# Performance work log

Measured on AMD Instinct MI355X. Metric: run time of the kernel, lower is better.

The kernel has to match this reference:

```python
import jax, jax.numpy as jnp
import numpy as np

V = 49152   # HEALPix nside=64 sphere: 12*64^2 vertices
B = 16      # batch of maps
DEG = 8     # avg neighbors per vertex
NNZ = V * DEG


def setup_inputs() -> dict:
    key = jax.random.key(0)
    ks = jax.random.split(key, 12)
    x = jax.random.normal(ks[0], (B, V, 1), jnp.float32)
    # COO sparse Laplacian (row-sorted)
    edge_row = jnp.repeat(jnp.arange(V, dtype=jnp.int32), DEG)
    edge_col = jax.random.randint(ks[1], (NNZ,), 0, V, dtype=jnp.int32)
    edge_w = jax.random.normal(ks[2], (NNZ,), jnp.float32) * 0.1

    def w(k, K, fi, fo):
        scale = 1.0 / np.sqrt(fi * K)
        return jax.random.normal(k, (K, fi, fo), jnp.float32) * scale

    return dict(
        x=x, edge_row=edge_row, edge_col=edge_col, edge_w=edge_w,
        w1=w(ks[3], 3, 1, 16),  b1=jnp.zeros((16,), jnp.float32),
        w2=w(ks[4], 3, 16, 64), b2=jnp.zeros((64,), jnp.float32),
        w3=w(ks[5], 3, 64, 16), b3=jnp.zeros((16,), jnp.float32),
        w4=w(ks[6], 1, 16, 1),  b4=jnp.zeros((1,), jnp.float32),
    )


def _spmm(edge_row, edge_col, edge_w, x_vbf):
    # sparse Laplacian @ x ; x_vbf: [V, B, F]
    msg = edge_w[:, None, None] * x_vbf[edge_col]          # [nnz, B, F]
    return jax.ops.segment_sum(msg, edge_row, num_segments=x_vbf.shape[0])


def _cheb_conv(edge_row, edge_col, edge_w, x_vbf, W, b):
    # Chebyshev recursion: x0 = x, x1 = L x, xk = 2 L x_{k-1} - x_{k-2}
    K = W.shape[0]
    xs = [x_vbf]
    if K > 1:
        xs.append(_spmm(edge_row, edge_col, edge_w, x_vbf))
        for _ in range(2, K):
            xs.append(2.0 * _spmm(edge_row, edge_col, edge_w, xs[-1]) - xs[-2])
    xk = jnp.stack(xs)                                     # [K, V, B, Fin]
    return jnp.einsum('kvbi,kio->vbo', xk, W) + b          # [V, B, Fout]


def reference(x, edge_row, edge_col, edge_w, w1, b1, w2, b2, w3, b3, w4, b4):
    h = jnp.transpose(x, (1, 0, 2))                        # [V, B, 1]
    h = jax.nn.relu(_cheb_conv(edge_row, edge_col, edge_w, h, w1, b1))
    h = jax.nn.relu(_cheb_conv(edge_row, edge_col, edge_w, h, w2, b2))
    h = jax.nn.relu(_cheb_conv(edge_row, edge_col, edge_w, h, w3, b3))
    h = _cheb_conv(edge_row, edge_col, edge_w, h, w4, b4)  # K=1 pointwise
    return jnp.transpose(h, (1, 0, 2))                     # [B, V, 1]
```

## Files before the change

kernel.cpp:

```cpp
#include <hip/hip_runtime.h>

#define V_N 49152
#define B_N 16
#define DEG 8

typedef __bf16 bf16x8 __attribute__((ext_vector_type(8)));
typedef __bf16 bf16x4 __attribute__((ext_vector_type(4)));
typedef __bf16 bf16x2 __attribute__((ext_vector_type(2)));
typedef float f32x4 __attribute__((ext_vector_type(4)));


template <int G>
__global__ __launch_bounds__(256) void k_transpose_g(const float* __restrict__ x,
                                                     float* __restrict__ xT, int b0) {
    int idx = blockIdx.x * 256 + threadIdx.x;
    int g = idx / V_N, v = idx - g * V_N;
    xT[v * G + g] = x[(b0 + g) * V_N + v];
}

template <int G>
__global__ __launch_bounds__(256) void k_spmm_g(const float* __restrict__ xin,
                                                const int* __restrict__ col,
                                                const float* __restrict__ ew,
                                                float* __restrict__ xout) {
    int idx = blockIdx.x * 256 + threadIdx.x;
    int v = idx / G, b = idx - v * G;
    const int e0 = v * DEG;
    float acc = 0.f;
#pragma unroll
    for (int e = 0; e < DEG; ++e)
        acc = fmaf(ew[e0 + e], xin[col[e0 + e] * G + b], acc);
    xout[idx] = acc;
}

template <int W4>
__global__ __launch_bounds__(256) void k_spmm_v(const float* __restrict__ xin,
                                                const int* __restrict__ col,
                                                const float* __restrict__ ew,
                                                float* __restrict__ xout) {
    int idx = blockIdx.x * 256 + threadIdx.x;
    int v = idx / W4;
    int c = (idx - v * W4) * 4;
    const int e0 = v * DEG;
    float4 acc = make_float4(0.f, 0.f, 0.f, 0.f);
#pragma unroll
    for (int e = 0; e < DEG; ++e) {
        float wv = ew[e0 + e];
        const float4 u = *(const float4*)&xin[(size_t)col[e0 + e] * (W4 * 4) + c];
        acc.x = fmaf(wv, u.x, acc.x);
        acc.y = fmaf(wv, u.y, acc.y);
        acc.z = fmaf(wv, u.z, acc.z);
        acc.w = fmaf(wv, u.w, acc.w);
    }
    *(float4*)&xout[(size_t)v * (W4 * 4) + c] = acc;
}

template <int W4>
__global__ __launch_bounds__(256) void k_spmm_vs(const float* __restrict__ xin,
                                                 int in_stride,
                                                 const int* __restrict__ col,
                                                 const float* __restrict__ ew,
                                                 float* __restrict__ xout,
                                                 int out_stride) {
    int idx = blockIdx.x * 256 + threadIdx.x;
    int v = idx / W4;
    int c = (idx - v * W4) * 4;
    const int e0 = v * DEG;
    float4 acc = make_float4(0.f, 0.f, 0.f, 0.f);
#pragma unroll
    for (int e = 0; e < DEG; ++e) {
        float wv = ew[e0 + e];
        const float4 u = *(const float4*)&xin[(size_t)col[e0 + e] * in_stride + c];
        acc.x = fmaf(wv, u.x, acc.x);
        acc.y = fmaf(wv, u.y, acc.y);
        acc.z = fmaf(wv, u.z, acc.z);
        acc.w = fmaf(wv, u.w, acc.w);
    }
    *(float4*)&xout[(size_t)v * out_stride + c] = acc;
}

template <int G>
__global__ __launch_bounds__(256) void k_fused1_g(const float* __restrict__ x0,
                                                  const float* __restrict__ x1,
                                                  const int* __restrict__ col,
                                                  const float* __restrict__ ew,
                                                  const float* __restrict__ W,
                                                  const float* __restrict__ bias,
                                                  float* __restrict__ out) {
    int idx = blockIdx.x * 256 + threadIdx.x;
    int v = idx / G;
    float a0 = x0[idx], a1 = x1[idx];
    const int e0 = v * DEG;
    float acc = 0.f;
#pragma unroll
    for (int e = 0; e < DEG; ++e)
        acc = fmaf(ew[e0 + e], x1[col[e0 + e] * G + (idx - v * G)], acc);
    float a2 = 2.f * acc - a0;
    float4* dst = (float4*)&out[(size_t)idx * 16];
#pragma unroll
    for (int oq = 0; oq < 4; ++oq) {
        float4 r;
        float* rp = (float*)&r;
#pragma unroll
        for (int j = 0; j < 4; ++j) {
            int o = oq * 4 + j;
            rp[j] = fmaxf(fmaf(a0, W[o], fmaf(a1, W[16 + o], fmaf(a2, W[32 + o], bias[o]))), 0.f);
        }
        dst[oq] = r;
    }
}

__global__ __launch_bounds__(256) void k_fused1_gb(const float* __restrict__ x0,
                                                   const float* __restrict__ x1,
                                                   const int* __restrict__ col,
                                                   const float* __restrict__ ew,
                                                   const float* __restrict__ W,
                                                   const float* __restrict__ bias,
                                                   float* __restrict__ out,
                                                   __bf16* __restrict__ outb) {
    int idx = blockIdx.x * 256 + threadIdx.x;
    int v = idx >> 3;
    float a0 = x0[idx], a1 = x1[idx];
    const int e0 = v * DEG;
    float acc = 0.f;
#pragma unroll
    for (int e = 0; e < DEG; ++e)
        acc = fmaf(ew[e0 + e], x1[col[e0 + e] * 8 + (idx & 7)], acc);
    float a2 = 2.f * acc - a0;
    float4* dst = (float4*)&out[(size_t)idx * 16];
    bf16x4* dstb = (bf16x4*)&outb[(size_t)idx * 16];
#pragma unroll
    for (int oq = 0; oq < 4; ++oq) {
        float4 r;
        float* rp = (float*)&r;
        bf16x4 rb;
#pragma unroll
        for (int j = 0; j < 4; ++j) {
            int o = oq * 4 + j;
            float h = fmaxf(fmaf(a0, W[o], fmaf(a1, W[16 + o], fmaf(a2, W[32 + o], bias[o]))), 0.f);
            rp[j] = h;
            rb[j] = (__bf16)h;
        }
        dst[oq] = r;
        dstb[oq] = rb;
    }
}

__global__ __launch_bounds__(256) void k_spmm_f2b(const __bf16* __restrict__ xin,
                                                  const int* __restrict__ col,
                                                  const float* __restrict__ ew,
                                                  __bf16* __restrict__ xout) {
    int idx = blockIdx.x * 256 + threadIdx.x;
    int v = idx >> 4;
    int c = (idx & 15) * 8;
    const int e0 = v * DEG;
    float acc[8];
#pragma unroll
    for (int j = 0; j < 8; ++j) acc[j] = 0.f;
#pragma unroll
    for (int e = 0; e < DEG; ++e) {
        float wv = ew[e0 + e];
        bf16x8 p = *(const bf16x8*)&xin[(size_t)col[e0 + e] * 128 + c];
#pragma unroll
        for (int j = 0; j < 8; ++j) acc[j] = fmaf(wv, (float)p[j], acc[j]);
    }
    bf16x8 o;
#pragma unroll
    for (int j = 0; j < 8; ++j) o[j] = (__bf16)acc[j];
    *(bf16x8*)&xout[(size_t)v * 128 + c] = o;
}

__global__ __launch_bounds__(256) void k_spmm_u(const __bf16* __restrict__ y1,
                                                const __bf16* __restrict__ y2,
                                                const int* __restrict__ col,
                                                const float* __restrict__ ew,
                                                __bf16* __restrict__ u) {
    int idx = blockIdx.x * 256 + threadIdx.x;
    int v = idx >> 4;
    int c = (idx & 15) * 8;
    const int e0 = v * DEG;
    float acc[8];
#pragma unroll
    for (int j = 0; j < 8; ++j) acc[j] = 0.f;
#pragma unroll
    for (int e = 0; e < DEG; ++e) {
        float wv = ew[e0 + e];
        bf16x8 p = *(const bf16x8*)&y2[(size_t)col[e0 + e] * 128 + c];
#pragma unroll
        for (int j = 0; j < 8; ++j) acc[j] = fmaf(wv, (float)p[j], acc[j]);
    }
    bf16x8 a = *(const bf16x8*)&y1[(size_t)v * 128 + c];
    bf16x8 o;
#pragma unroll
    for (int j = 0; j < 8; ++j) o[j] = (__bf16)fmaf(2.f, acc[j], (float)a[j]);
    *(bf16x8*)&u[(size_t)v * 128 + c] = o;
}

__global__ __launch_bounds__(512) void k_prepack(const float* __restrict__ w2,
                                                 const float* __restrict__ w3,
                                                 __bf16* __restrict__ pk) {
    int t = threadIdx.x;
    {
        int kt = t >> 8, nt = (t >> 6) & 3, lane = t & 63;
#pragma unroll
        for (int e = 0; e < 8; ++e) {
            int k = kt * 32 + ((lane >> 4) * 8) + e;
            float val = (k < 48) ? w2[(k >> 4) * 1024 + (k & 15) * 64 + nt * 16 + (lane & 15)] : 0.f;
            __bf16 hi = (__bf16)val;
            pk[t * 8 + e] = hi;
            pk[4096 + t * 8 + e] = (__bf16)(val - (float)hi);
        }
    }
    if (t < 384) {
        int kt = t / 192, nt = (t / 64) % 3, lane = t & 63;
#pragma unroll
        for (int e = 0; e < 8; ++e) {
            int k = kt * 32 + ((lane >> 4) * 8) + e;
            float val = w3[nt * 1024 + k * 16 + (lane & 15)];
            __bf16 hi = (__bf16)val;
            pk[8192 + t * 8 + e] = hi;
            pk[11264 + t * 8 + e] = (__bf16)(val - (float)hi);
        }
    }
}

__global__ __launch_bounds__(256) void k_fused2y_mfma(const float* __restrict__ x0,
                                                      const __bf16* __restrict__ x1,
                                                      const int* __restrict__ col,
                                                      const float* __restrict__ ew,
                                                      const __bf16* __restrict__ pk,
                                                      const float* __restrict__ b2,
                                                      float* __restrict__ y02,
                                                      __bf16* __restrict__ y1o,
                                                      __bf16* __restrict__ y2o) {
    __shared__ __attribute__((aligned(16))) __bf16 s_hi[4][16 * 72];
    __shared__ __attribute__((aligned(16))) __bf16 s_lo[4][16 * 72];
    __shared__ int   sc[8][8];
    __shared__ float sw[8][8];
    const int t = threadIdx.x;
    const int v0 = blockIdx.x * 8;
    if (t < 64) {
        int vl = t >> 3, e = t & 7;
        sc[vl][e] = col[(v0 + vl) * DEG + e];
        sw[vl][e] = ew[(v0 + vl) * DEG + e];
    }
    __syncthreads();
    for (int u = t; u < 512; u += 256) {
        int tile = u >> 7, row = (u >> 3) & 15, i = (u & 7) * 2;
        bf16x2 z; z[0] = (__bf16)0.f; z[1] = (__bf16)0.f;
        *(bf16x2*)&s_hi[tile][row * 72 + 48 + i] = z;
        *(bf16x2*)&s_lo[tile][row * 72 + 48 + i] = z;
    }
    const int su = t * 4;
    const int svl = su >> 7, sel = su & 127;
    const int stile = svl >> 1;
    const int srow = (svl & 1) * 8 + (sel >> 4);
    const int skbase = srow * 72 + (sel & 15);
    const size_t srowg = (size_t)(v0 + svl) * 128;
    {
        float4 val = *(const float4*)&x0[srowg + sel];
        const float* vp = (const float*)&val;
        bf16x4 hi4, lo4;
#pragma unroll
        for (int j = 0; j < 4; ++j) {
            __bf16 h = (__bf16)vp[j];
            hi4[j] = h;
            lo4[j] = (__bf16)(vp[j] - (float)h);
        }
        *(bf16x4*)&s_hi[stile][skbase] = hi4;
        *(bf16x4*)&s_lo[stile][skbase] = lo4;
    }
    {
        bf16x4 hi4 = *(const bf16x4*)&x1[srowg + sel];
        bf16x4 lo4;
#pragma unroll
        for (int j = 0; j < 4; ++j) lo4[j] = (__bf16)0.f;
        *(bf16x4*)&s_hi[stile][skbase + 16] = hi4;
        *(bf16x4*)&s_lo[stile][skbase + 16] = lo4;
    }
    {
        float a[4] = {0.f, 0.f, 0.f, 0.f};
#pragma unroll
        for (int e = 0; e < DEG; ++e) {
            float wv = sw[svl][e];
            bf16x4 p = *(const bf16x4*)&x1[(size_t)sc[svl][e] * 128 + sel];
#pragma unroll
            for (int j = 0; j < 4; ++j) a[j] = fmaf(wv, (float)p[j], a[j]);
        }
        float4 val = *(const float4*)&x0[srowg + sel];
        const float* vp = (const float*)&val;
        bf16x4 hi4, lo4;
#pragma unroll
        for (int j = 0; j < 4; ++j) {
            float vx = 2.f * a[j] - vp[j];
            __bf16 h = (__bf16)vx;
            hi4[j] = h;
            lo4[j] = (__bf16)(vx - (float)h);
        }
        *(bf16x4*)&s_hi[stile][skbase + 32] = hi4;
        *(bf16x4*)&s_lo[stile][skbase + 32] = lo4;
    }
    __syncthreads();
    const int wv = t >> 6, lane = t & 63;
    const int lrow = lane & 15, lkg = lane >> 4;
    f32x4 acc[4] = {{0.f,0.f,0.f,0.f},{0.f,0.f,0.f,0.f},{0.f,0.f,0.f,0.f},{0.f,0.f,0.f,0.f}};
#pragma unroll
    for (int kt = 0; kt < 2; ++kt) {
        bf16x8 Ah = *(const bf16x8*)&s_hi[wv][lrow * 72 + kt * 32 + lkg * 8];
        bf16x8 Al = *(const bf16x8*)&s_lo[wv][lrow * 72 + kt * 32 + lkg * 8];
#pragma unroll
        for (int nt = 0; nt < 4; ++nt) {
            bf16x8 Wh = *(const bf16x8*)&pk[((kt * 4 + nt) * 64 + lane) * 8];
            bf16x8 Wl = *(const bf16x8*)&pk[4096 + ((kt * 4 + nt) * 64 + lane) * 8];
            acc[nt] = __builtin_amdgcn_mfma_f32_16x16x32_bf16(Ah, Wh, acc[nt], 0, 0, 0);
            acc[nt] = __builtin_amdgcn_mfma_f32_16x16x32_bf16(Al, Wh, acc[nt], 0, 0, 0);
            acc[nt] = __builtin_amdgcn_mfma_f32_16x16x32_bf16(Ah, Wl, acc[nt], 0, 0, 0);
        }
    }
    __builtin_amdgcn_sched_barrier(0);
#pragma unroll
    for (int nt = 0; nt < 4; ++nt) {
        float bias = b2[nt * 16 + lrow];
#pragma unroll
        for (int r = 0; r < 4; ++r) {
            int row = lkg * 4 + r;
            float h = fmaxf(acc[nt][r] + bias, 0.f);
            __bf16 hh = (__bf16)h;
            s_hi[wv][row * 72 + nt * 16 + lrow] = hh;
            s_lo[wv][row * 72 + nt * 16 + lrow] = (__bf16)(h - (float)hh);
        }
    }
    f32x4 accy[3] = {{0.f,0.f,0.f,0.f},{0.f,0.f,0.f,0.f},{0.f,0.f,0.f,0.f}};
#pragma unroll
    for (int kt = 0; kt < 2; ++kt) {
        bf16x8 Ah = *(const bf16x8*)&s_hi[wv][lrow * 72 + kt * 32 + lkg * 8];
        bf16x8 Al = *(const bf16x8*)&s_lo[wv][lrow * 72 + kt * 32 + lkg * 8];
#pragma unroll
        for (int nt = 0; nt < 3; ++nt) {
            bf16x8 Wh = *(const bf16x8*)&pk[8192 + ((kt * 3 + nt) * 64 + lane) * 8];
            bf16x8 Wl = *(const bf16x8*)&pk[11264 + ((kt * 3 + nt) * 64 + lane) * 8];
            accy[nt] = __builtin_amdgcn_mfma_f32_16x16x32_bf16(Ah, Wh, accy[nt], 0, 0, 0);
            accy[nt] = __builtin_amdgcn_mfma_f32_16x16x32_bf16(Al, Wh, accy[nt], 0, 0, 0);
            accy[nt] = __builtin_amdgcn_mfma_f32_16x16x32_bf16(Ah, Wl, accy[nt], 0, 0, 0);
        }
    }
    const int vbase = v0 + wv * 2;
#pragma unroll
    for (int r = 0; r < 4; ++r) {
        int row = lkg * 4 + r;
        int v = vbase + (row >> 3), g = row & 7;
        size_t off = (size_t)v * 128 + g * 16 + lrow;
        y02[off] = accy[0][r] - accy[2][r];
        y1o[off] = (__bf16)accy[1][r];
        y2o[off] = (__bf16)accy[2][r];
    }
}

__global__ __launch_bounds__(256) void k_final_gb(const float* __restrict__ y02,
                                                  const __bf16* __restrict__ u,
                                                  const int* __restrict__ col,
                                                  const float* __restrict__ ew,
                                                  const float* __restrict__ b3,
                                                  const float* __restrict__ w4,
                                                  const float* __restrict__ b4,
                                                  float* __restrict__ out, int b0) {
    int idx = blockIdx.x * 256 + threadIdx.x;
    int v = idx >> 3, g = idx & 7;
    const int e0 = v * DEG;
    float acc[16];
#pragma unroll
    for (int j = 0; j < 16; ++j) acc[j] = 0.f;
#pragma unroll
    for (int e = 0; e < DEG; ++e) {
        float wv = ew[e0 + e];
        const __bf16* src = u + (size_t)col[e0 + e] * 128 + g * 16;
        bf16x8 u0 = *(const bf16x8*)src;
        bf16x8 u1 = *(const bf16x8*)(src + 8);
#pragma unroll
        for (int j = 0; j < 8; ++j) {
            acc[j] = fmaf(wv, (float)u0[j], acc[j]);
            acc[8 + j] = fmaf(wv, (float)u1[j], acc[8 + j]);
        }
    }
    const float4* yp = (const float4*)&y02[(size_t)v * 128 + g * 16];
    float r = b4[0];
#pragma unroll
    for (int q = 0; q < 4; ++q) {
        float4 yv = yp[q];
        const float* py = (const float*)&yv;
#pragma unroll
        for (int j = 0; j < 4; ++j) {
            float h = py[j] + acc[q * 4 + j] + b3[q * 4 + j];
            h = fmaxf(h, 0.f);
            r = fmaf(h, w4[q * 4 + j], r);
        }
    }
    out[(b0 + g) * V_N + v] = r;
}

template <int G>
__global__ __launch_bounds__(256) void k_fused2y(const float* __restrict__ x0,
                                                 const float* __restrict__ x1,
                                                 const int* __restrict__ col,
                                                 const float* __restrict__ ew,
                                                 const float* __restrict__ W2,
                                                 const float* __restrict__ b2,
                                                 const float* __restrict__ W3,
                                                 float* __restrict__ y) {
    constexpr int R = 16 * G;
    __shared__ float s[4][3 * R];
    __shared__ float sh2[4][G][64];
    __shared__ float sW2[3072];
    __shared__ float sW3[3072];
    __shared__ float sB[64];
    __shared__ int   sc[4][DEG];
    __shared__ float sw[4][DEG];
    const int t = threadIdx.x;
    const int v0 = blockIdx.x * 4;
    for (int j = t; j < 3072; j += 256) { sW2[j] = W2[j]; sW3[j] = W3[j]; }
    if (t < 64) sB[t] = b2[t];
    if (t < 32) {
        int vl = t >> 3, e = t & 7;
        sc[vl][e] = col[(v0 + vl) * DEG + e];
        sw[vl][e] = ew[(v0 + vl) * DEG + e];
    }
    __syncthreads();
    for (int u = t; u < 4 * R; u += 256) {
        int vl = u / R, el = u - vl * R;
        size_t row = (size_t)(v0 + vl) * R;
        float a0 = x0[row + el];
        float a1 = x1[row + el];
        s[vl][0 * R + el] = a0;
        s[vl][1 * R + el] = a1;
        float acc = 0.f;
#pragma unroll
        for (int e = 0; e < DEG; ++e)
            acc = fmaf(sw[vl][e], x1[(size_t)sc[vl][e] * R + el], acc);
        s[vl][2 * R + el] = 2.f * acc - a0;
    }
    __syncthreads();
    const int vl = t >> 6, o = t & 63;
    float wc[48];
#pragma unroll
    for (int k = 0; k < 3; ++k)
#pragma unroll
        for (int i = 0; i < 16; ++i)
            wc[k * 16 + i] = sW2[k * 1024 + i * 64 + o];
    float bias = sB[o];
#pragma unroll
    for (int g = 0; g < G; ++g) {
        float r = bias;
#pragma unroll
        for (int k = 0; k < 3; ++k) {
            const float4* ap = (const float4*)&s[vl][k * R + g * 16];
#pragma unroll
            for (int iq = 0; iq < 4; ++iq) {
                float4 a = ap[iq];
                r = fmaf(a.x, wc[k * 16 + iq * 4 + 0], r);
                r = fmaf(a.y, wc[k * 16 + iq * 4 + 1], r);
                r = fmaf(a.z, wc[k * 16 + iq * 4 + 2], r);
                r = fmaf(a.w, wc[k * 16 + iq * 4 + 3], r);
            }
        }
        sh2[vl][g][o] = fmaxf(r, 0.f);
    }
    __syncthreads();
    if (o < 48) {
        const int k3 = o >> 4, o3 = o & 15;
        float wy[64];
#pragma unroll
        for (int i = 0; i < 64; ++i)
            wy[i] = sW3[k3 * 1024 + i * 16 + o3];
        size_t yrow = (size_t)(v0 + vl) * (48 * G) + (size_t)k3 * (16 * G) + o3;
#pragma unroll
        for (int g = 0; g < G; ++g) {
            float r = 0.f;
            const float4* hp = (const float4*)&sh2[vl][g][0];
#pragma unroll
            for (int iq = 0; iq < 16; ++iq) {
                float4 h = hp[iq];
                r = fmaf(h.x, wy[iq * 4 + 0], r);
                r = fmaf(h.y, wy[iq * 4 + 1], r);
                r = fmaf(h.z, wy[iq * 4 + 2], r);
                r = fmaf(h.w, wy[iq * 4 + 3], r);
            }
            y[yrow + (size_t)g * 16] = r;
        }
    }
}

template <int G>
__global__ __launch_bounds__(256) void k_final_g(const float* __restrict__ y,
                                                 const float* __restrict__ z,
                                                 const int* __restrict__ col,
                                                 const float* __restrict__ ew,
                                                 const float* __restrict__ b3,
                                                 const float* __restrict__ w4,
                                                 const float* __restrict__ b4,
                                                 float* __restrict__ out, int b0) {
    int idx = blockIdx.x * 256 + threadIdx.x;
    int v = idx / G, g = idx - v * G;
    const size_t yr = (size_t)v * (48 * G) + g * 16;
    const size_t zr = (size_t)v * (32 * G) + g * 16;
    const int e0 = v * DEG;
    float4 acc[4];
#pragma unroll
    for (int q = 0; q < 4; ++q) acc[q] = make_float4(0.f, 0.f, 0.f, 0.f);
#pragma unroll
    for (int e = 0; e < DEG; ++e) {
        float wv = ew[e0 + e];
        const float* src = z + (size_t)col[e0 + e] * (32 * G) + 16 * G + g * 16;
#pragma unroll
        for (int q = 0; q < 4; ++q) {
            float4 u = *(const float4*)(src + q * 4);
            acc[q].x = fmaf(wv, u.x, acc[q].x);
            acc[q].y = fmaf(wv, u.y, acc[q].y);
            acc[q].z = fmaf(wv, u.z, acc[q].z);
            acc[q].w = fmaf(wv, u.w, acc[q].w);
        }
    }
    float r = b4[0];
#pragma unroll
    for (int q = 0; q < 4; ++q) {
        float4 y0v = *(const float4*)(y + yr + q * 4);
        float4 y2v = *(const float4*)(y + yr + (size_t)32 * G + q * 4);
        float4 z1v = *(const float4*)(z + zr + q * 4);
        const float* a = (const float*)&acc[q];
        const float* p0 = (const float*)&y0v;
        const float* p2 = (const float*)&y2v;
        const float* p1 = (const float*)&z1v;
#pragma unroll
        for (int j = 0; j < 4; ++j) {
            float h = p0[j] - p2[j] + p1[j] + 2.f * a[j] + b3[q * 4 + j];
            h = fmaxf(h, 0.f);
            r = fmaf(h, w4[q * 4 + j], r);
        }
    }
    out[(b0 + g) * V_N + v] = r;
}

template <int G>
static void run_pipeline(const float* x, const int* ecol, const float* ew,
                         const float* w1, const float* b1, const float* w2, const float* b2,
                         const float* w3, const float* b3, const float* w4, const float* b4,
                         float* out, float* ws, hipStream_t stream) {
    const size_t V = V_N;
    dim3 blk(256);
    if constexpr (G == 8) {
        float*  xT  = ws;
        float*  x1  = xT + 8 * V;
        float*  h1  = x1 + 8 * V;
        __bf16* h1b = (__bf16*)(h1 + 128 * V);
        __bf16* x1b = (__bf16*)(h1 + 192 * V);
        float*  y02 = h1 + 256 * V;
        __bf16* y1b = (__bf16*)(y02 + 128 * V);
        __bf16* y2b = y1b + 128 * V;
        __bf16* ub  = x1b;
        __bf16* pk  = (__bf16*)(h1 + 512 * V);
        k_prepack<<<1, 512, 0, stream>>>(w2, w3, pk);
        for (int b0 = 0; b0 < B_N; b0 += 8) {
            k_transpose_g<8><<<(V * 8) / 256, blk, 0, stream>>>(x, xT, b0);
            k_spmm_g<8><<<(V * 8) / 256, blk, 0, stream>>>(xT, ecol, ew, x1);
            k_fused1_gb<<<(V * 8) / 256, blk, 0, stream>>>(xT, x1, ecol, ew, w1, b1, h1, h1b);
            k_spmm_f2b<<<(V * 16) / 256, blk, 0, stream>>>(h1b, ecol, ew, x1b);
            k_fused2y_mfma<<<V / 8, blk, 0, stream>>>(h1, x1b, ecol, ew, pk, b2, y02, y1b, y2b);
            k_spmm_u<<<(V * 16) / 256, blk, 0, stream>>>(y1b, y2b, ecol, ew, ub);
            k_final_gb<<<(V * 8) / 256, blk, 0, stream>>>(y02, ub, ecol, ew, b3, w4, b4, out, b0);
        }
    } else {
        const size_t GV = (size_t)G * V;
        float* xT   = ws;
        float* x1   = xT + GV;
        float* h1   = x1 + GV;
        float* x1b  = h1 + 16 * GV;
        float* y012 = x1b + 16 * GV;
        float* z12  = h1;
        for (int b0 = 0; b0 < B_N; b0 += G) {
            k_transpose_g<G><<<(V * G) / 256, blk, 0, stream>>>(x, xT, b0);
            k_spmm_g<G><<<(V * G) / 256, blk, 0, stream>>>(xT, ecol, ew, x1);
            k_fused1_g<G><<<(V * G) / 256, blk, 0, stream>>>(xT, x1, ecol, ew, w1, b1, h1);
            k_spmm_v<4 * G><<<(V * 4 * G) / 256, blk, 0, stream>>>(h1, ecol, ew, x1b);
            k_fused2y<G><<<V / 4, blk, 0, stream>>>(h1, x1b, ecol, ew, w2, b2, w3, y012);
            k_spmm_vs<8 * G><<<(V * 8 * G) / 256, blk, 0, stream>>>(
                y012 + 16 * G, 48 * G, ecol, ew, z12, 32 * G);
            k_final_g<G><<<(V * G) / 256, blk, 0, stream>>>(y012, z12, ecol, ew, b3, w4, b4, out, b0);
        }
    }
}

extern "C" void kernel_launch(void* const* d_in, const int* in_sizes, int n_in,
                              void* d_out, int out_size, void* d_ws, size_t ws_size,
                              hipStream_t stream) {
    const float* x = (const float*)d_in[0];
    const int* ecol = (const int*)d_in[2];
    const float* ew = (const float*)d_in[3];
    const float* w1 = (const float*)d_in[4];
    const float* b1 = (const float*)d_in[5];
    const float* w2 = (const float*)d_in[6];
    const float* b2 = (const float*)d_in[7];
    const float* w3 = (const float*)d_in[8];
    const float* b3 = (const float*)d_in[9];
    const float* w4 = (const float*)d_in[10];
    const float* b4 = (const float*)d_in[11];
    float* out = (float*)d_out;
    float* ws = (float*)d_ws;

    auto need = [](int G) { return (size_t)82 * G * V_N * 4; };
    if (ws_size >= need(8))
        run_pipeline<8>(x, ecol, ew, w1, b1, w2, b2, w3, b3, w4, b4, out, ws, stream);
    else if (ws_size >= need(4))
        run_pipeline<4>(x, ecol, ew, w1, b1, w2, b2, w3, b3, w4, b4, out, ws, stream);
    else if (ws_size >= need(2))
        run_pipeline<2>(x, ecol, ew, w1, b1, w2, b2, w3, b3, w4, b4, out, ws, stream);
    else
        run_pipeline<1>(x, ecol, ew, w1, b1, w2, b2, w3, b3, w4, b4, out, ws, stream);
}
```

Before: 233.3 us.

## Process both batch groups per launch and store y02 in bf16

The pipeline now handles two groups of 8 batch maps in a single set of launches when the workspace allows, indexing a second vertex range offset by V. This halves the number of kernel launches and doubles the grid size of each. The y02 intermediate is stored in bf16 instead of fp32 to cut memory traffic, and y1 reuses the h1b buffer. The fallback pipelines for G<8 are removed, and the bf16 storage of y02 adds rounding error.

Result: faster. 207.2 us (-11.2%).

```diff
diff --git a/kernel.cpp b/kernel.cpp
--- a/kernel.cpp
+++ b/kernel.cpp
@@ -10,104 +10,28 @@
 typedef float f32x4 __attribute__((ext_vector_type(4)));
 
 
-template <int G>
-__global__ __launch_bounds__(256) void k_transpose_g(const float* __restrict__ x,
-                                                     float* __restrict__ xT, int b0) {
-    int idx = blockIdx.x * 256 + threadIdx.x;
-    int g = idx / V_N, v = idx - g * V_N;
-    xT[v * G + g] = x[(b0 + g) * V_N + v];
-}
-
-template <int G>
-__global__ __launch_bounds__(256) void k_spmm_g(const float* __restrict__ xin,
-                                                const int* __restrict__ col,
-                                                const float* __restrict__ ew,
-                                                float* __restrict__ xout) {
-    int idx = blockIdx.x * 256 + threadIdx.x;
-    int v = idx / G, b = idx - v * G;
-    const int e0 = v * DEG;
-    float acc = 0.f;
-#pragma unroll
-    for (int e = 0; e < DEG; ++e)
-        acc = fmaf(ew[e0 + e], xin[col[e0 + e] * G + b], acc);
-    xout[idx] = acc;
-}
-
-template <int W4>
-__global__ __launch_bounds__(256) void k_spmm_v(const float* __restrict__ xin,
-                                                const int* __restrict__ col,
-                                                const float* __restrict__ ew,
-                                                float* __restrict__ xout) {
-    int idx = blockIdx.x * 256 + threadIdx.x;
-    int v = idx / W4;
-    int c = (idx - v * W4) * 4;
-    const int e0 = v * DEG;
-    float4 acc = make_float4(0.f, 0.f, 0.f, 0.f);
-#pragma unroll
-    for (int e = 0; e < DEG; ++e) {
-        float wv = ew[e0 + e];
-        const float4 u = *(const float4*)&xin[(size_t)col[e0 + e] * (W4 * 4) + c];
-        acc.x = fmaf(wv, u.x, acc.x);
-        acc.y = fmaf(wv, u.y, acc.y);
-        acc.z = fmaf(wv, u.z, acc.z);
-        acc.w = fmaf(wv, u.w, acc.w);
-    }
-    *(float4*)&xout[(size_t)v * (W4 * 4) + c] = acc;
-}
-
-template <int W4>
-__global__ __launch_bounds__(256) void k_spmm_vs(const float* __restrict__ xin,
-                                                 int in_stride,
+__global__ __launch_bounds__(256) void k_transpose(const float* __restrict__ x,
+                                                   float* __restrict__ xT, int b0) {
+    int idx = blockIdx.x * 256 + threadIdx.x;
+    int v = idx % V_N, bg = idx / V_N;
+    xT[((size_t)(bg >> 3) * V_N + v) * 8 + (bg & 7)] = x[(size_t)(b0 + bg) * V_N + v];
+}
+
+__global__ __launch_bounds__(256) void k_spmm_g8(const float* __restrict__ xin,
                                                  const int* __restrict__ col,
                                                  const float* __restrict__ ew,
-                                                 float* __restrict__ xout,
-                                                 int out_stride) {
-    int idx = blockIdx.x * 256 + threadIdx.x;
-    int v = idx / W4;
-    int c = (idx - v * W4) * 4;
-    const int e0 = v * DEG;
-    float4 acc = make_float4(0.f, 0.f, 0.f, 0.f);
-#pragma unroll
-    for (int e = 0; e < DEG; ++e) {
-        float wv = ew[e0 + e];
-        const float4 u = *(const float4*)&xin[(size_t)col[e0 + e] * in_stride + c];
-        acc.x = fmaf(wv, u.x, acc.x);
-        acc.y = fmaf(wv, u.y, acc.y);
-        acc.z = fmaf(wv, u.z, acc.z);
-        acc.w = fmaf(wv, u.w, acc.w);
-    }
-    *(float4*)&xout[(size_t)v * out_stride + c] = acc;
-}
-
-template <int G>
-__global__ __launch_bounds__(256) void k_fused1_g(const float* __restrict__ x0,
-                                                  const float* __restrict__ x1,
-                                                  const int* __restrict__ col,
-                                                  const float* __restrict__ ew,
-                                                  const float* __restrict__ W,
-                                                  const float* __restrict__ bias,
-                                                  float* __restrict__ out) {
-    int idx = blockIdx.x * 256 + threadIdx.x;
-    int v = idx / G;
-    float a0 = x0[idx], a1 = x1[idx];
+                                                 float* __restrict__ xout) {
+    int idx = blockIdx.x * 256 + threadIdx.x;
+    int vv = idx >> 3, b = idx & 7;
+    int grp = vv >= V_N;
+    int v = vv - (grp ? V_N : 0);
+    int goff = grp ? V_N : 0;
     const int e0 = v * DEG;
     float acc = 0.f;
 #pragma unroll
     for (int e = 0; e < DEG; ++e)
-        acc = fmaf(ew[e0 + e], x1[col[e0 + e] * G + (idx - v * G)], acc);
-    float a2 = 2.f * acc - a0;
-    float4* dst = (float4*)&out[(size_t)idx * 16];
-#pragma unroll
-    for (int oq = 0; oq < 4; ++oq) {
-        float4 r;
-        float* rp = (float*)&r;
-#pragma unroll
-        for (int j = 0; j < 4; ++j) {
-            int o = oq * 4 + j;
-            rp[j] = fmaxf(fmaf(a0, W[o], fmaf(a1, W[16 + o], fmaf(a2, W[32 + o], bias[o]))), 0.f);
-        }
-        dst[oq] = r;
-    }
+        acc = fmaf(ew[e0 + e], xin[(size_t)(goff + col[e0 + e]) * 8 + b], acc);
+    xout[idx] = acc;
 }
 
 __global__ __launch_bounds__(256) void k_fused1_gb(const float* __restrict__ x0,
@@ -119,13 +43,16 @@
                                                    float* __restrict__ out,
                                                    __bf16* __restrict__ outb) {
     int idx = blockIdx.x * 256 + threadIdx.x;
-    int v = idx >> 3;
+    int vv = idx >> 3, g = idx & 7;
+    int grp = vv >= V_N;
+    int v = vv - (grp ? V_N : 0);
+    int goff = grp ? V_N : 0;
     float a0 = x0[idx], a1 = x1[idx];
     const int e0 = v * DEG;
     float acc = 0.f;
 #pragma unroll
     for (int e = 0; e < DEG; ++e)
-        acc = fmaf(ew[e0 + e], x1[col[e0 + e] * 8 + (idx & 7)], acc);
+        acc = fmaf(ew[e0 + e], x1[(size_t)(goff + col[e0 + e]) * 8 + g], acc);
     float a2 = 2.f * acc - a0;
     float4* dst = (float4*)&out[(size_t)idx * 16];
     bf16x4* dstb = (bf16x4*)&outb[(size_t)idx * 16];
@@ -151,8 +78,11 @@
                                                   const float* __restrict__ ew,
                                                   __bf16* __restrict__ xout) {
     int idx = blockIdx.x * 256 + threadIdx.x;
-    int v = idx >> 4;
+    int vv = idx >> 4;
     int c = (idx & 15) * 8;
+    int grp = vv >= V_N;
+    int v = vv - (grp ? V_N : 0);
+    int goff = grp ? V_N : 0;
     const int e0 = v * DEG;
     float acc[8];
 #pragma unroll
@@ -160,14 +90,14 @@
 #pragma unroll
     for (int e = 0; e < DEG; ++e) {
         float wv = ew[e0 + e];
-        bf16x8 p = *(const bf16x8*)&xin[(size_t)col[e0 + e] * 128 + c];
+        bf16x8 p = *(const bf16x8*)&xin[(size_t)(goff + col[e0 + e]) * 128 + c];
 #pragma unroll
         for (int j = 0; j < 8; ++j) acc[j] = fmaf(wv, (float)p[j], acc[j]);
     }
     bf16x8 o;
 #pragma unroll
     for (int j = 0; j < 8; ++j) o[j] = (__bf16)acc[j];
-    *(bf16x8*)&xout[(size_t)v * 128 + c] = o;
+    *(bf16x8*)&xout[(size_t)vv * 128 + c] = o;
 }
 
 __global__ __launch_bounds__(256) void k_spmm_u(const __bf16* __restrict__ y1,
@@ -176,8 +106,11 @@
                                                 const float* __restrict__ ew,
                                                 __bf16* __restrict__ u) {
     int idx = blockIdx.x * 256 + threadIdx.x;
-    int v = idx >> 4;
+    int vv = idx >> 4;
     int c = (idx & 15) * 8;
+    int grp = vv >= V_N;
+    int v = vv - (grp ? V_N : 0);
+    int goff = grp ? V_N : 0;
     const int e0 = v * DEG;
     float acc[8];
 #pragma unroll
@@ -185,15 +118,15 @@
 #pragma unroll
     for (int e = 0; e < DEG; ++e) {
         float wv = ew[e0 + e];
-        bf16x8 p = *(const bf16x8*)&y2[(size_t)col[e0 + e] * 128 + c];
+        bf16x8 p = *(const bf16x8*)&y2[(size_t)(goff + col[e0 + e]) * 128 + c];
 #pragma unroll
         for (int j = 0; j < 8; ++j) acc[j] = fmaf(wv, (float)p[j], acc[j]);
     }
-    bf16x8 a = *(const bf16x8*)&y1[(size_t)v * 128 + c];
+    bf16x8 a = *(const bf16x8*)&y1[(size_t)vv * 128 + c];
     bf16x8 o;
 #pragma unroll
     for (int j = 0; j < 8; ++j) o[j] = (__bf16)fmaf(2.f, acc[j], (float)a[j]);
-    *(bf16x8*)&u[(size_t)v * 128 + c] = o;
+    *(bf16x8*)&u[(size_t)vv * 128 + c] = o;
 }
 
 __global__ __launch_bounds__(512) void k_prepack(const float* __restrict__ w2,
@@ -230,7 +163,7 @@
                                                       const float* __restrict__ ew,
                                                       const __bf16* __restrict__ pk,
                                                       const float* __restrict__ b2,
-                                                      float* __restrict__ y02,
+                                                      __bf16* __restrict__ y02o,
                                                       __bf16* __restrict__ y1o,
                                                       __bf16* __restrict__ y2o) {
     __shared__ __attribute__((aligned(16))) __bf16 s_hi[4][16 * 72];
@@ -239,10 +172,13 @@
     __shared__ float sw[8][8];
     const int t = threadIdx.x;
     const int v0 = blockIdx.x * 8;
+    const int grp = v0 >= V_N;
+    const int vloc = v0 - (grp ? V_N : 0);
+    const int goff = grp ? V_N : 0;
     if (t < 64) {
         int vl = t >> 3, e = t & 7;
-        sc[vl][e] = col[(v0 + vl) * DEG + e];
-        sw[vl][e] = ew[(v0 + vl) * DEG + e];
+        sc[vl][e] = goff + col[(vloc + vl) * DEG + e];
+        sw[vl][e] = ew[(vloc + vl) * DEG + e];
     }
     __syncthreads();
     for (int u = t; u < 512; u += 256) {
@@ -350,13 +286,13 @@
         int row = lkg * 4 + r;
         int v = vbase + (row >> 3), g = row & 7;
         size_t off = (size_t)v * 128 + g * 16 + lrow;
-        y02[off] = accy[0][r] - accy[2][r];
+        y02o[off] = (__bf16)(accy[0][r] - accy[2][r]);
         y1o[off] = (__bf16)accy[1][r];
         y2o[off] = (__bf16)accy[2][r];
     }
 }
 
-__global__ __launch_bounds__(256) void k_final_gb(const float* __restrict__ y02,
+__global__ __launch_bounds__(256) void k_final_gb(const __bf16* __restrict__ y02,
                                                   const __bf16* __restrict__ u,
                                                   const int* __restrict__ col,
                                                   const float* __restrict__ ew,
@@ -365,7 +301,10 @@
                                                   const float* __restrict__ b4,
                                                   float* __restrict__ out, int b0) {
     int idx = blockIdx.x * 256 + threadIdx.x;
-    int v = idx >> 3, g = idx & 7;
+    int vv = idx >> 3, g = idx & 7;
+    int grp = vv >= V_N;
+    int v = vv - (grp ? V_N : 0);
+    int goff = grp ? V_N : 0;
     const int e0 = v * DEG;
     float acc[16];
 #pragma unroll
@@ -373,7 +312,7 @@
 #pragma unroll
     for (int e = 0; e < DEG; ++e) {
         float wv = ew[e0 + e];
-        const __bf16* src = u + (size_t)col[e0 + e] * 128 + g * 16;
+        const __bf16* src = u + (size_t)(goff + col[e0 + e]) * 128 + g * 16;
         bf16x8 u0 = *(const bf16x8*)src;
         bf16x8 u1 = *(const bf16x8*)(src + 8);
 #pragma unroll
@@ -382,210 +321,18 @@
             acc[8 + j] = fmaf(wv, (float)u1[j], acc[8 + j]);
         }
     }
-    const float4* yp = (const float4*)&y02[(size_t)v * 128 + g * 16];
+    const __bf16* yp = y02 + (size_t)vv * 128 + g * 16;
+    bf16x8 y0v = *(const bf16x8*)yp;
+    bf16x8 y1v = *(const bf16x8*)(yp + 8);
     float r = b4[0];
 #pragma unroll
-    for (int q = 0; q < 4; ++q) {
-        float4 yv = yp[q];
-        const float* py = (const float*)&yv;
-#pragma unroll
-        for (int j = 0; j < 4; ++j) {
-            float h = py[j] + acc[q * 4 + j] + b3[q * 4 + j];
-            h = fmaxf(h, 0.f);
-            r = fmaf(h, w4[q * 4 + j], r);
-        }
-    }
-    out[(b0 + g) * V_N + v] = r;
-}
-
-template <int G>
-__global__ __launch_bounds__(256) void k_fused2y(const float* __restrict__ x0,
-                                                 const float* __restrict__ x1,
-                                                 const int* __restrict__ col,
-                                                 const float* __restrict__ ew,
-                                                 const float* __restrict__ W2,
-                                                 const float* __restrict__ b2,
-                                                 const float* __restrict__ W3,
-                                                 float* __restrict__ y) {
-    constexpr int R = 16 * G;
-    __shared__ float s[4][3 * R];
-    __shared__ float sh2[4][G][64];
-    __shared__ float sW2[3072];
-    __shared__ float sW3[3072];
-    __shared__ float sB[64];
-    __shared__ int   sc[4][DEG];
-    __shared__ float sw[4][DEG];
-    const int t = threadIdx.x;
-    const int v0 = blockIdx.x * 4;
-    for (int j = t; j < 3072; j += 256) { sW2[j] = W2[j]; sW3[j] = W3[j]; }
-    if (t < 64) sB[t] = b2[t];
-    if (t < 32) {
-        int vl = t >> 3, e = t & 7;
-        sc[vl][e] = col[(v0 + vl) * DEG + e];
-        sw[vl][e] = ew[(v0 + vl) * DEG + e];
-    }
-    __syncthreads();
-    for (int u = t; u < 4 * R; u += 256) {
-        int vl = u / R, el = u - vl * R;
-        size_t row = (size_t)(v0 + vl) * R;
-        float a0 = x0[row + el];
-        float a1 = x1[row + el];
-        s[vl][0 * R + el] = a0;
-        s[vl][1 * R + el] = a1;
-        float acc = 0.f;
-#pragma unroll
-        for (int e = 0; e < DEG; ++e)
-            acc = fmaf(sw[vl][e], x1[(size_t)sc[vl][e] * R + el], acc);
-        s[vl][2 * R + el] = 2.f * acc - a0;
-    }
-    __syncthreads();
-    const int vl = t >> 6, o = t & 63;
-    float wc[48];
-#pragma unroll
-    for (int k = 0; k < 3; ++k)
-#pragma unroll
-        for (int i = 0; i < 16; ++i)
-            wc[k * 16 + i] = sW2[k * 1024 + i * 64 + o];
-    float bias = sB[o];
-#pragma unroll
-    for (int g = 0; g < G; ++g) {
-        float r = bias;
-#pragma unroll
-        for (int k = 0; k < 3; ++k) {
-            const float4* ap = (const float4*)&s[vl][k * R + g * 16];
-#pragma unroll
-            for (int iq = 0; iq < 4; ++iq) {
-                float4 a = ap[iq];
-                r = fmaf(a.x, wc[k * 16 + iq * 4 + 0], r);
-                r = fmaf(a.y, wc[k * 16 + iq * 4 + 1], r);
-                r = fmaf(a.z, wc[k * 16 + iq * 4 + 2], r);
-                r = fmaf(a.w, wc[k * 16 + iq * 4 + 3], r);
-            }
-        }
-        sh2[vl][g][o] = fmaxf(r, 0.f);
-    }
-    __syncthreads();
-    if (o < 48) {
-        const int k3 = o >> 4, o3 = o & 15;
-        float wy[64];
-#pragma unroll
-        for (int i = 0; i < 64; ++i)
-            wy[i] = sW3[k3 * 1024 + i * 16 + o3];
-        size_t yrow = (size_t)(v0 + vl) * (48 * G) + (size_t)k3 * (16 * G) + o3;
-#pragma unroll
-        for (int g = 0; g < G; ++g) {
-            float r = 0.f;
-            const float4* hp = (const float4*)&sh2[vl][g][0];
-#pragma unroll
-            for (int iq = 0; iq < 16; ++iq) {
-                float4 h = hp[iq];
-                r = fmaf(h.x, wy[iq * 4 + 0], r);
-                r = fmaf(h.y, wy[iq * 4 + 1], r);
-                r = fmaf(h.z, wy[iq * 4 + 2], r);
-                r = fmaf(h.w, wy[iq * 4 + 3], r);
-            }
-            y[yrow + (size_t)g * 16] = r;
-        }
-    }
-}
-
-template <int G>
-__global__ __launch_bounds__(256) void k_final_g(const float* __restrict__ y,
-                                                 const float* __restrict__ z,
-                                                 const int* __restrict__ col,
-                                                 const float* __restrict__ ew,
-                                                 const float* __restrict__ b3,
-                                                 const float* __restrict__ w4,
-                                                 const float* __restrict__ b4,
-                                                 float* __restrict__ out, int b0) {
-    int idx = blockIdx.x * 256 + threadIdx.x;
-    int v = idx / G, g = idx - v * G;
-    const size_t yr = (size_t)v * (48 * G) + g * 16;
-    const size_t zr = (size_t)v * (32 * G) + g * 16;
-    const int e0 = v * DEG;
-    float4 acc[4];
-#pragma unroll
-    for (int q = 0; q < 4; ++q) acc[q] = make_float4(0.f, 0.f, 0.f, 0.f);
-#pragma unroll
-    for (int e = 0; e < DEG; ++e) {
-        float wv = ew[e0 + e];
-        const float* src = z + (size_t)col[e0 + e] * (32 * G) + 16 * G + g * 16;
-#pragma unroll
-        for (int q = 0; q < 4; ++q) {
-            float4 u = *(const float4*)(src + q * 4);
-            acc[q].x = fmaf(wv, u.x, acc[q].x);
-            acc[q].y = fmaf(wv, u.y, acc[q].y);
-            acc[q].z = fmaf(wv, u.z, acc[q].z);
-            acc[q].w = fmaf(wv, u.w, acc[q].w);
-        }
-    }
-    float r = b4[0];
-#pragma unroll
-    for (int q = 0; q < 4; ++q) {
-        float4 y0v = *(const float4*)(y + yr + q * 4);
-        float4 y2v = *(const float4*)(y + yr + (size_t)32 * G + q * 4);
-        float4 z1v = *(const float4*)(z + zr + q * 4);
-        const float* a = (const float*)&acc[q];
-        const float* p0 = (const float*)&y0v;
-        const float* p2 = (const float*)&y2v;
-        const float* p1 = (const float*)&z1v;
-#pragma unroll
-        for (int j = 0; j < 4; ++j) {
-            float h = p0[j] - p2[j] + p1[j] + 2.f * a[j] + b3[q * 4 + j];
-            h = fmaxf(h, 0.f);
-            r = fmaf(h, w4[q * 4 + j], r);
-        }
-    }
-    out[(b0 + g) * V_N + v] = r;
-}
-
-template <int G>
-static void run_pipeline(const float* x, const int* ecol, const float* ew,
-                         const float* w1, const float* b1, const float* w2, const float* b2,
-                         const float* w3, const float* b3, const float* w4, const float* b4,
-                         float* out, float* ws, hipStream_t stream) {
-    const size_t V = V_N;
-    dim3 blk(256);
-    if constexpr (G == 8) {
-        float*  xT  = ws;
-        float*  x1  = xT + 8 * V;
-        float*  h1  = x1 + 8 * V;
-        __bf16* h1b = (__bf16*)(h1 + 128 * V);
-        __bf16* x1b = (__bf16*)(h1 + 192 * V);
-        float*  y02 = h1 + 256 * V;
-        __bf16* y1b = (__bf16*)(y02 + 128 * V);
-        __bf16* y2b = y1b + 128 * V;
-        __bf16* ub  = x1b;
-        __bf16* pk  = (__bf16*)(h1 + 512 * V);
-        k_prepack<<<1, 512, 0, stream>>>(w2, w3, pk);
-        for (int b0 = 0; b0 < B_N; b0 += 8) {
-            k_transpose_g<8><<<(V * 8) / 256, blk, 0, stream>>>(x, xT, b0);
-            k_spmm_g<8><<<(V * 8) / 256, blk, 0, stream>>>(xT, ecol, ew, x1);
-            k_fused1_gb<<<(V * 8) / 256, blk, 0, stream>>>(xT, x1, ecol, ew, w1, b1, h1, h1b);
-            k_spmm_f2b<<<(V * 16) / 256, blk, 0, stream>>>(h1b, ecol, ew, x1b);
-            k_fused2y_mfma<<<V / 8, blk, 0, stream>>>(h1, x1b, ecol, ew, pk, b2, y02, y1b, y2b);
-            k_spmm_u<<<(V * 16) / 256, blk, 0, stream>>>(y1b, y2b, ecol, ew, ub);
-            k_final_gb<<<(V * 8) / 256, blk, 0, stream>>>(y02, ub, ecol, ew, b3, w4, b4, out, b0);
-        }
-    } else {
-        const size_t GV = (size_t)G * V;
-        float* xT   = ws;
-        float* x1   = xT + GV;
-        float* h1   = x1 + GV;
-        float* x1b  = h1 + 16 * GV;
-        float* y012 = x1b + 16 * GV;
-        float* z12  = h1;
-        for (int b0 = 0; b0 < B_N; b0 += G) {
-            k_transpose_g<G><<<(V * G) / 256, blk, 0, stream>>>(x, xT, b0);
-            k_spmm_g<G><<<(V * G) / 256, blk, 0, stream>>>(xT, ecol, ew, x1);
-            k_fused1_g<G><<<(V * G) / 256, blk, 0, stream>>>(xT, x1, ecol, ew, w1, b1, h1);
-            k_spmm_v<4 * G><<<(V * 4 * G) / 256, blk, 0, stream>>>(h1, ecol, ew, x1b);
-            k_fused2y<G><<<V / 4, blk, 0, stream>>>(h1, x1b, ecol, ew, w2, b2, w3, y012);
-            k_spmm_vs<8 * G><<<(V * 8 * G) / 256, blk, 0, stream>>>(
-                y012 + 16 * G, 48 * G, ecol, ew, z12, 32 * G);
-            k_final_g<G><<<(V * G) / 256, blk, 0, stream>>>(y012, z12, ecol, ew, b3, w4, b4, out, b0);
-        }
-    }
+    for (int j = 0; j < 8; ++j) {
+        float h = fmaxf((float)y0v[j] + acc[j] + b3[j], 0.f);
+        r = fmaf(h, w4[j], r);
+        float h2 = fmaxf((float)y1v[j] + acc[8 + j] + b3[8 + j], 0.f);
+        r = fmaf(h2, w4[8 + j], r);
+    }
+    out[(size_t)(b0 + grp * 8 + g) * V_N + v] = r;
 }
 
 extern "C" void kernel_launch(void* const* d_in, const int* in_sizes, int n_in,
@@ -605,13 +352,31 @@
     float* out = (float*)d_out;
     float* ws = (float*)d_ws;
 
-    auto need = [](int G) { return (size_t)82 * G * V_N * 4; };
-    if (ws_size >= need(8))
-        run_pipeline<8>(x, ecol, ew, w1, b1, w2, b2, w3, b3, w4, b4, out, ws, stream);
-    else if (ws_size >= need(4))
-        run_pipeline<4>(x, ecol, ew, w1, b1, w2, b2, w3, b3, w4, b4, out, ws, stream);
-    else if (ws_size >= need(2))
-        run_pipeline<2>(x, ecol, ew, w1, b1, w2, b2, w3, b3, w4, b4, out, ws, stream);
-    else
-        run_pipeline<1>(x, ecol, ew, w1, b1, w2, b2, w3, b3, w4, b4, out, ws, stream);
-}
+    const size_t V = V_N;
+    const size_t need2 = (size_t)(800 * V + 8192) * 4;
+    const int NB = (ws_size >= need2) ? 2 : 1;
+    const size_t VR = (size_t)NB * V;
+
+    float*  xT   = ws;
+    float*  x1   = xT + 8 * VR;
+    float*  h1   = x1 + 8 * VR;
+    __bf16* h1b  = (__bf16*)(h1 + 128 * VR);
+    __bf16* x1b  = (__bf16*)(h1 + 192 * VR);
+    __bf16* y02b = (__bf16*)(h1 + 256 * VR);
+    __bf16* y2b  = (__bf16*)(h1 + 320 * VR);
+    __bf16* y1b  = h1b;
+    __bf16* ub   = x1b;
+    __bf16* pk   = (__bf16*)(h1 + 384 * VR);
+
+    dim3 blk(256);
+    k_prepack<<<1, 512, 0, stream>>>(w2, w3, pk);
+    for (int b0 = 0; b0 < B_N; b0 += NB * 8) {
+        k_transpose<<<(VR * 8) / 256, blk, 0, stream>>>(x, xT, b0);
+        k_spmm_g8<<<(VR * 8) / 256, blk, 0, stream>>>(xT, ecol, ew, x1);
+        k_fused1_gb<<<(VR * 8) / 256, blk, 0, stream>>>(xT, x1, ecol, ew, w1, b1, h1, h1b);
+        k_spmm_f2b<<<(VR * 16) / 256, blk, 0, stream>>>(h1b, ecol, ew, x1b);
+        k_fused2y_mfma<<<VR / 8, blk, 0, stream>>>(h1, x1b, ecol, ew, pk, b2, y02b, y1b, y2b);
+        k_spmm_u<<<(VR * 16) / 256, blk, 0, stream>>>(y1b, y2b, ecol, ew, ub);
+        k_final_gb<<<(VR * 8) / 256, blk, 0, stream>>>(y02b, ub, ecol, ew, b3, w4, b4, out, b0);
+    }
+}
```
